# Performance work log

Hardware: AMD Instinct MI355X
Metric: run time of the kernel (lower is better)

## Reference

```python
import jax, jax.numpy as jnp
import numpy as np

NUM_NODES = 100000
NUM_EDGES = 1600000
NUM_GRAPHS = 64
IN_DIM, HID, NCLS = 64, 128, 10


def setup_inputs() -> dict:
    key = jax.random.key(0)
    ks = jax.random.split(key, 12)
    x = jax.random.normal(ks[0], (NUM_NODES, IN_DIM), dtype=jnp.float32)
    src = jax.random.randint(ks[1], (NUM_EDGES,), 0, NUM_NODES, dtype=jnp.int32)
    dst = jax.random.randint(ks[2], (NUM_EDGES,), 0, NUM_NODES, dtype=jnp.int32)
    batch = jnp.sort(jax.random.randint(ks[3], (NUM_NODES,), 0, NUM_GRAPHS, dtype=jnp.int32))
    def glorot(k, shape):
        lim = (6.0 / (shape[0] + shape[1])) ** 0.5
        return jax.random.uniform(k, shape, jnp.float32, -lim, lim)
    return {
        "x": x, "src": src, "dst": dst, "batch": batch,
        "W1": glorot(ks[4], (IN_DIM, HID)), "b1": jnp.zeros((HID,), jnp.float32),
        "W2": glorot(ks[5], (HID, HID)), "b2": jnp.zeros((HID,), jnp.float32),
        "Wl1": glorot(ks[6], (HID, HID // 2)), "bl1": jnp.zeros((HID // 2,), jnp.float32),
        "Wl2": glorot(ks[7], (HID // 2, NCLS)), "bl2": jnp.zeros((NCLS,), jnp.float32),
    }


def gcn_conv(x, W, b, src, dst):
    # GCNConv: out = D^{-1/2} (A + I) D^{-1/2} (x @ W) + b, deg from A+I
    h = x @ W  # [N, H]
    ones = jnp.ones((src.shape[0],), h.dtype)
    deg = jax.ops.segment_sum(ones, dst, num_segments=NUM_NODES) + 1.0  # +1 self-loop
    dinv = jax.lax.rsqrt(deg)  # [N]
    norm = dinv[src] * dinv[dst]  # [E]
    msg = h[src] * norm[:, None]  # [E, H] gather + scale
    agg = jax.ops.segment_sum(msg, dst, num_segments=NUM_NODES)  # scatter-add
    agg = agg + h * (dinv * dinv)[:, None]  # self-loop message
    return agg + b


def reference(x, src, dst, batch, W1, b1, W2, b2, Wl1, bl1, Wl2, bl2):
    h = jax.nn.relu(gcn_conv(x, W1, b1, src, dst))
    h = jax.nn.relu(gcn_conv(h, W2, b2, src, dst))
    # global mean pool per graph
    sums = jax.ops.segment_sum(h, batch, num_segments=NUM_GRAPHS)  # [G, H]
    cnts = jax.ops.segment_sum(jnp.ones((h.shape[0],), h.dtype), batch, num_segments=NUM_GRAPHS)
    pooled = sums / jnp.maximum(cnts, 1.0)[:, None]
    h = jax.nn.relu(pooled @ Wl1 + bl1)
    return h @ Wl2 + bl2  # [G, num_classes]
```

## Files before the change

kernel.cpp:

```cpp
#include <hip/hip_runtime.h>
#include <hip/hip_bf16.h>

#define NODES_N 100000
#define EDGES_E 1600000
#define GRAPHS_G 64

#define BIN_SHIFT 7
#define BIN_NODES 128
#define NBINS 782
#define NB1 512
#define EPB1 3125

typedef unsigned int uint;
typedef unsigned short ushort;
typedef __attribute__((ext_vector_type(8))) short bf16x8;
typedef __attribute__((ext_vector_type(4))) float f32x4;


__device__ inline uint pack_bf2(float lo, float hi) {
    __hip_bfloat162 h2 = __float22bfloat162_rn(make_float2(lo, hi));
    return *reinterpret_cast<uint*>(&h2);
}

__device__ inline void acc_bf2(uint w, float& a0, float& a1) {
    a0 += __uint_as_float(w << 16);
    a1 += __uint_as_float(w & 0xffff0000u);
}

__device__ inline ushort f2bf(float v) {
    __hip_bfloat16 b = __float2bfloat16(v);
    return *reinterpret_cast<ushort*>(&b);
}


__device__ inline void pack_w_one(const float* W, ushort* Wf, int gid, int KS) {
    int j = gid & 7, l = (gid >> 3) & 63, f = gid >> 9;
    int nt = f / KS, ks = f - nt * KS;
    int k = ks * 32 + ((l >> 4) & 3) * 8 + j;
    int n = nt * 16 + (l & 15);
    Wf[gid] = f2bf(W[k * 128 + n]);
}

#define NZERO (GRAPHS_G * 128 + GRAPHS_G)

__global__ void pack_w_zero_k(const float* __restrict__ W1, ushort* __restrict__ W1f,
                              const float* __restrict__ W2, ushort* __restrict__ W2f,
                              float* __restrict__ zf) {
    int gid = blockIdx.x * 256 + threadIdx.x;
    if (gid < 8192) pack_w_one(W1, W1f, gid, 2);
    else if (gid < 24576) pack_w_one(W2, W2f, gid - 8192, 4);
    else {
        int i = gid - 24576;
        if (i < NZERO) zf[i] = 0.f;
    }
}


__global__ __launch_bounds__(256) void p1_hist_k(const int* __restrict__ dst,
                                                 int* __restrict__ hist_t) {
    __shared__ int h[NBINS];
    for (int i = threadIdx.x; i < NBINS; i += 256) h[i] = 0;
    __syncthreads();
    int b = blockIdx.x;
    int e0 = b * EPB1, e1 = min(EDGES_E, e0 + EPB1);
    for (int e = e0 + threadIdx.x; e < e1; e += 256)
        atomicAdd(&h[dst[e] >> BIN_SHIFT], 1);
    __syncthreads();
    for (int i = threadIdx.x; i < NBINS; i += 256)
        hist_t[i * NB1 + b] = h[i];
}

__global__ __launch_bounds__(256) void p1_scanbins_k(int* __restrict__ hist_t,
                                                     int* __restrict__ bintot) {
    __shared__ int sd[256];
    __shared__ int carry;
    int bin = blockIdx.x, t = threadIdx.x;
    if (t == 0) carry = 0;
    __syncthreads();
    int* row = hist_t + bin * NB1;
    for (int base = 0; base < NB1; base += 256) {
        int v = row[base + t];
        sd[t] = v; __syncthreads();
        for (int o = 1; o < 256; o <<= 1) {
            int x = (t >= o) ? sd[t - o] : 0;
            __syncthreads();
            sd[t] += x;
            __syncthreads();
        }
        row[base + t] = carry + sd[t] - v;
        __syncthreads();
        if (t == 255) carry += sd[255];
        __syncthreads();
    }
    if (t == 0) bintot[bin] = carry;
}

__global__ __launch_bounds__(1024) void binstart_k(const int* __restrict__ bintot,
                                                   int* __restrict__ binstart,
                                                   int* __restrict__ rowptr) {
    __shared__ int sd[1024];
    int t = threadIdx.x;
    int v = (t < NBINS) ? bintot[t] : 0;
    sd[t] = v; __syncthreads();
    for (int o = 1; o < 1024; o <<= 1) {
        int x = (t >= o) ? sd[t - o] : 0;
        __syncthreads();
        sd[t] += x;
        __syncthreads();
    }
    if (t < NBINS) binstart[t] = sd[t] - v;
    if (t == 0) { binstart[NBINS] = EDGES_E; rowptr[NODES_N] = EDGES_E; }
}

__global__ __launch_bounds__(256) void p1_scatter_k(const int* __restrict__ src,
                                                    const int* __restrict__ dst,
                                                    const int* __restrict__ hist_t,
                                                    const int* __restrict__ binstart,
                                                    uint* __restrict__ pairs) {
    __shared__ int cur[NBINS];
    int b = blockIdx.x;
    for (int i = threadIdx.x; i < NBINS; i += 256)
        cur[i] = binstart[i] + hist_t[i * NB1 + b];
    __syncthreads();
    int e0 = b * EPB1, e1 = min(EDGES_E, e0 + EPB1);
    for (int e = e0 + threadIdx.x; e < e1; e += 256) {
        int d = dst[e];
        int pos = atomicAdd(&cur[d >> BIN_SHIFT], 1);
        pairs[pos] = ((uint)src[e] << BIN_SHIFT) | (uint)(d & (BIN_NODES - 1));
    }
}

__global__ __launch_bounds__(256) void p2_build_k(const uint* __restrict__ pairs,
                                                  const int* __restrict__ binstart,
                                                  const float* __restrict__ x,
                                                  int* __restrict__ colidx,
                                                  int* __restrict__ rowptr,
                                                  float* __restrict__ dinv,
                                                  uint* __restrict__ xt) {
    __shared__ int h[BIN_NODES];
    __shared__ int off[BIN_NODES];
    __shared__ int cur[BIN_NODES];
    __shared__ float ldv[BIN_NODES];
    int bin = blockIdx.x, t = threadIdx.x;
    int node0 = bin << BIN_SHIFT;
    if (t < BIN_NODES) h[t] = 0;
    __syncthreads();
    int e0 = binstart[bin], e1 = binstart[bin + 1];
    for (int e = e0 + t; e < e1; e += 256)
        atomicAdd(&h[pairs[e] & (BIN_NODES - 1)], 1);
    __syncthreads();
    if (t < BIN_NODES) off[t] = h[t];
    __syncthreads();
    for (int o = 1; o < BIN_NODES; o <<= 1) {
        int x2 = (t < BIN_NODES && t >= o) ? off[t - o] : 0;
        __syncthreads();
        if (t < BIN_NODES) off[t] += x2;
        __syncthreads();
    }
    if (t < BIN_NODES) {
        int excl = off[t] - h[t];
        cur[t] = e0 + excl;
        float dv = rsqrtf((float)h[t] + 1.0f);
        ldv[t] = dv;
        int node = node0 + t;
        if (node < NODES_N) {
            rowptr[node] = e0 + excl;
            dinv[node] = dv;
        }
    }
    __syncthreads();
    for (int e = e0 + t; e < e1; e += 256) {
        uint p = pairs[e];
        int pos = atomicAdd(&cur[p & (BIN_NODES - 1)], 1);
        colidx[pos] = (int)(p >> BIN_SHIFT);
    }
    int nmax = min(NODES_N - node0, BIN_NODES);
    for (int i = t; i < nmax * 16; i += 256) {
        int nl = i >> 4, c = i & 15;
        int node = node0 + nl;
        float dv = ldv[nl];
        float4 v = *(const float4*)&x[(size_t)node * 64 + c * 4];
        uint2 o = make_uint2(pack_bf2(v.x * dv, v.y * dv), pack_bf2(v.z * dv, v.w * dv));
        *(uint2*)&xt[(size_t)node * 32 + c * 2] = o;
    }
}


__global__ __launch_bounds__(256) void gather64_k(const uint* __restrict__ xt,
                                                  const int* __restrict__ rowptr,
                                                  const int* __restrict__ colidx,
                                                  uint* __restrict__ st, int n) {
    int lane = threadIdx.x & 7;
    int local = threadIdx.x >> 3;
    int co = lane * 4;
    int node = blockIdx.x * 32 + local;
    if (node >= n) return;
    {
        float a0=0,a1=0,a2=0,a3=0,a4=0,a5=0,a6=0,a7=0;
        uint4 v = *(const uint4*)&xt[(size_t)node * 32 + co];
        acc_bf2(v.x, a0, a1); acc_bf2(v.y, a2, a3);
        acc_bf2(v.z, a4, a5); acc_bf2(v.w, a6, a7);
        int beg = rowptr[node], end = rowptr[node + 1];
        int e = beg;
        for (; e + 3 < end; e += 4) {
            int s0 = colidx[e], s1 = colidx[e+1], s2 = colidx[e+2], s3 = colidx[e+3];
            uint4 v0 = *(const uint4*)&xt[(size_t)s0 * 32 + co];
            uint4 v1 = *(const uint4*)&xt[(size_t)s1 * 32 + co];
            uint4 v2 = *(const uint4*)&xt[(size_t)s2 * 32 + co];
            uint4 v3 = *(const uint4*)&xt[(size_t)s3 * 32 + co];
            acc_bf2(v0.x,a0,a1); acc_bf2(v0.y,a2,a3); acc_bf2(v0.z,a4,a5); acc_bf2(v0.w,a6,a7);
            acc_bf2(v1.x,a0,a1); acc_bf2(v1.y,a2,a3); acc_bf2(v1.z,a4,a5); acc_bf2(v1.w,a6,a7);
            acc_bf2(v2.x,a0,a1); acc_bf2(v2.y,a2,a3); acc_bf2(v2.z,a4,a5); acc_bf2(v2.w,a6,a7);
            acc_bf2(v3.x,a0,a1); acc_bf2(v3.y,a2,a3); acc_bf2(v3.z,a4,a5); acc_bf2(v3.w,a6,a7);
        }
        for (; e < end; e++) {
            uint4 v0 = *(const uint4*)&xt[(size_t)colidx[e] * 32 + co];
            acc_bf2(v0.x,a0,a1); acc_bf2(v0.y,a2,a3); acc_bf2(v0.z,a4,a5); acc_bf2(v0.w,a6,a7);
        }
        uint4 o;
        o.x = pack_bf2(a0, a1);
        o.y = pack_bf2(a2, a3);
        o.z = pack_bf2(a4, a5);
        o.w = pack_bf2(a6, a7);
        *(uint4*)&st[(size_t)node * 32 + co] = o;
    }
}


__global__ __launch_bounds__(256) void gemm_dual_k(const ushort* __restrict__ A,
                                                   const ushort* __restrict__ W1f,
                                                   const ushort* __restrict__ W2f,
                                                   const float* __restrict__ dinv,
                                                   const float* __restrict__ b1,
                                                   ushort* __restrict__ h2p, int n) {
    __shared__ ushort hl[4][16][132];
    int wave = threadIdx.x >> 6;
    int lane = threadIdx.x & 63;
    int row0 = (blockIdx.x * 4 + wave) * 16;
    if (row0 >= n) return;
    int m = lane & 15, g = lane >> 4;
    int arow = min(row0 + m, n - 1);

    const ushort* ab = &A[(size_t)arow * 64 + g * 8];
    bf16x8 a0 = *reinterpret_cast<const bf16x8*>(ab);
    bf16x8 a1 = *reinterpret_cast<const bf16x8*>(ab + 32);
    f32x4 acc[8];
#pragma unroll
    for (int nt = 0; nt < 8; nt++) {
        acc[nt] = (f32x4){0.f, 0.f, 0.f, 0.f};
        bf16x8 w0 = *reinterpret_cast<const bf16x8*>(&W1f[((size_t)(nt * 2 + 0) * 64 + lane) * 8]);
        bf16x8 w1 = *reinterpret_cast<const bf16x8*>(&W1f[((size_t)(nt * 2 + 1) * 64 + lane) * 8]);
        acc[nt] = __builtin_amdgcn_mfma_f32_16x16x32_bf16(a0, w0, acc[nt], 0, 0, 0);
        acc[nt] = __builtin_amdgcn_mfma_f32_16x16x32_bf16(a1, w1, acc[nt], 0, 0, 0);
    }

    int orow0 = row0 + g * 4;
#pragma unroll
    for (int r = 0; r < 4; r++) {
        float dvr = dinv[min(orow0 + r, n - 1)];
#pragma unroll
        for (int nt = 0; nt < 8; nt++) {
            float v = fmaxf(fmaf(dvr, acc[nt][r], b1[nt * 16 + m]), 0.f);
            hl[wave][g * 4 + r][nt * 16 + m] = f2bf(v);
        }
    }

    bf16x8 hfrag[4];
#pragma unroll
    for (int ks = 0; ks < 4; ks++) {
        uint2 lo = *(const uint2*)&hl[wave][m][g * 8 + ks * 32];
        uint2 hi = *(const uint2*)&hl[wave][m][g * 8 + ks * 32 + 4];
        uint4 u = make_uint4(lo.x, lo.y, hi.x, hi.y);
        hfrag[ks] = *reinterpret_cast<bf16x8*>(&u);
    }

    f32x4 acc2[8];
#pragma unroll
    for (int nt = 0; nt < 8; nt++) {
        acc2[nt] = (f32x4){0.f, 0.f, 0.f, 0.f};
#pragma unroll
        for (int ks = 0; ks < 4; ks++) {
            bf16x8 w = *reinterpret_cast<const bf16x8*>(&W2f[((size_t)(nt * 4 + ks) * 64 + lane) * 8]);
            acc2[nt] = __builtin_amdgcn_mfma_f32_16x16x32_bf16(hfrag[ks], w, acc2[nt], 0, 0, 0);
        }
    }

#pragma unroll
    for (int r = 0; r < 4; r++) {
        int row = orow0 + r;
        if (row < n) {
            float dvr = dinv[row];
#pragma unroll
            for (int nt = 0; nt < 8; nt++)
                h2p[(size_t)row * 128 + nt * 16 + m] = f2bf(acc2[nt][r] * dvr);
        }
    }
}


__global__ __launch_bounds__(256) void gather128_k(const uint* __restrict__ hp,
                                                   const int* __restrict__ rowptr,
                                                   const int* __restrict__ colidx,
                                                   const float* __restrict__ dinv,
                                                   const float* __restrict__ bias,
                                                   uint* __restrict__ h2b, int n) {
    int P = blockIdx.y;
    int lane = threadIdx.x & 7;
    int local = threadIdx.x >> 3;
    int co = P * 32 + lane * 4;
    int node = blockIdx.x * 32 + local;
    if (node >= n) return;
    {
        float a0=0,a1=0,a2=0,a3=0,a4=0,a5=0,a6=0,a7=0;
        uint4 v = *(const uint4*)&hp[(size_t)node * 64 + co];
        acc_bf2(v.x, a0, a1); acc_bf2(v.y, a2, a3);
        acc_bf2(v.z, a4, a5); acc_bf2(v.w, a6, a7);
        int beg = rowptr[node], end = rowptr[node + 1];
        int e = beg;
        for (; e + 3 < end; e += 4) {
            int s0 = colidx[e], s1 = colidx[e+1], s2 = colidx[e+2], s3 = colidx[e+3];
            uint4 v0 = *(const uint4*)&hp[(size_t)s0 * 64 + co];
            uint4 v1 = *(const uint4*)&hp[(size_t)s1 * 64 + co];
            uint4 v2 = *(const uint4*)&hp[(size_t)s2 * 64 + co];
            uint4 v3 = *(const uint4*)&hp[(size_t)s3 * 64 + co];
            acc_bf2(v0.x,a0,a1); acc_bf2(v0.y,a2,a3); acc_bf2(v0.z,a4,a5); acc_bf2(v0.w,a6,a7);
            acc_bf2(v1.x,a0,a1); acc_bf2(v1.y,a2,a3); acc_bf2(v1.z,a4,a5); acc_bf2(v1.w,a6,a7);
            acc_bf2(v2.x,a0,a1); acc_bf2(v2.y,a2,a3); acc_bf2(v2.z,a4,a5); acc_bf2(v2.w,a6,a7);
            acc_bf2(v3.x,a0,a1); acc_bf2(v3.y,a2,a3); acc_bf2(v3.z,a4,a5); acc_bf2(v3.w,a6,a7);
        }
        for (; e < end; e++) {
            uint4 v0 = *(const uint4*)&hp[(size_t)colidx[e] * 64 + co];
            acc_bf2(v0.x,a0,a1); acc_bf2(v0.y,a2,a3); acc_bf2(v0.z,a4,a5); acc_bf2(v0.w,a6,a7);
        }
        float dv = dinv[node];
        int jb = P * 64 + lane * 8;
        float4 b0 = *(const float4*)&bias[jb];
        float4 b1 = *(const float4*)&bias[jb + 4];
        float o0 = fmaxf(fmaf(dv, a0, b0.x), 0.f);
        float o1 = fmaxf(fmaf(dv, a1, b0.y), 0.f);
        float o2 = fmaxf(fmaf(dv, a2, b0.z), 0.f);
        float o3 = fmaxf(fmaf(dv, a3, b0.w), 0.f);
        float o4 = fmaxf(fmaf(dv, a4, b1.x), 0.f);
        float o5 = fmaxf(fmaf(dv, a5, b1.y), 0.f);
        float o6 = fmaxf(fmaf(dv, a6, b1.z), 0.f);
        float o7 = fmaxf(fmaf(dv, a7, b1.w), 0.f);
        uint4 ov;
        ov.x = pack_bf2(o0, o1);
        ov.y = pack_bf2(o2, o3);
        ov.z = pack_bf2(o4, o5);
        ov.w = pack_bf2(o6, o7);
        *(uint4*)&h2b[(size_t)node * 64 + co] = ov;
    }
}


__global__ __launch_bounds__(128) void pool_k(const uint* __restrict__ h2b,
                                              const int* __restrict__ batch, int n,
                                              float* __restrict__ sums, float* __restrict__ cnts) {
    int j = threadIdx.x;
    int wj = j >> 1;
    int hi = j & 1;
    int chunk = (n + gridDim.x - 1) / gridDim.x;
    int i0 = blockIdx.x * chunk;
    int i1 = min(n, i0 + chunk);
    if (i0 >= n) return;
    int cur = batch[i0];
    float acc = 0.f;
    int cnt = 0;
    for (int i = i0; i < i1; i++) {
        int g = batch[i];
        if (g != cur) {
            atomicAdd(&sums[cur * 128 + j], acc);
            if (j == 0) atomicAdd(&cnts[cur], (float)cnt);
            acc = 0.f; cnt = 0; cur = g;
        }
        uint w = h2b[(size_t)i * 64 + wj];
        acc += __uint_as_float(hi ? (w & 0xffff0000u) : (w << 16));
        cnt++;
    }
    atomicAdd(&sums[cur * 128 + j], acc);
    if (j == 0) atomicAdd(&cnts[cur], (float)cnt);
}


__global__ __launch_bounds__(64) void mlp_k(const float* __restrict__ sums, const float* __restrict__ cnts,
                                            const float* __restrict__ Wl1, const float* __restrict__ bl1,
                                            const float* __restrict__ Wl2, const float* __restrict__ bl2,
                                            float* __restrict__ out) {
    __shared__ float pooled[128];
    __shared__ float hidden[64];
    int g = blockIdx.x, t = threadIdx.x;
    float c = fmaxf(cnts[g], 1.0f);
    pooled[t]      = sums[g * 128 + t] / c;
    pooled[t + 64] = sums[g * 128 + 64 + t] / c;
    __syncthreads();
    float a = bl1[t];
#pragma unroll 4
    for (int cc = 0; cc < 128; cc++) a = fmaf(pooled[cc], Wl1[cc * 64 + t], a);
    hidden[t] = fmaxf(a, 0.f);
    __syncthreads();
    if (t < 10) {
        float o = bl2[t];
#pragma unroll 8
        for (int jj = 0; jj < 64; jj++) o = fmaf(hidden[jj], Wl2[jj * 10 + t], o);
        out[g * 10 + t] = o;
    }
}


extern "C" void kernel_launch(void* const* d_in, const int* in_sizes, int n_in,
                              void* d_out, int out_size, void* d_ws, size_t ws_size,
                              hipStream_t stream) {
    const float* x    = (const float*)d_in[0];
    const int*   src  = (const int*)d_in[1];
    const int*   dst  = (const int*)d_in[2];
    const int*   batch= (const int*)d_in[3];
    const float* W1   = (const float*)d_in[4];
    const float* b1   = (const float*)d_in[5];
    const float* W2   = (const float*)d_in[6];
    const float* b2   = (const float*)d_in[7];
    const float* Wl1  = (const float*)d_in[8];
    const float* bl1  = (const float*)d_in[9];
    const float* Wl2  = (const float*)d_in[10];
    const float* bl2  = (const float*)d_in[11];
    float* out = (float*)d_out;

    const int N = NODES_N;

    size_t off = 0;
    auto take = [&](size_t bytes) { size_t o = off; off = (off + bytes + 255) & ~(size_t)255; return o; };
    char* ws = (char*)d_ws;
    uint*   h2p  = (uint*)(ws + take((size_t)N * 128 * 2));
    uint*   h2b  = (uint*)(ws + take((size_t)N * 128 * 2));
    size_t  shbytes = (size_t)N * 64 * 2;
    char*   shreg = ws + take(shbytes);
    uint*   pairs = (uint*)shreg;
    uint*   stil  = (uint*)shreg;
    uint*   xt   = (uint*)(ws + take((size_t)N * 64 * 2));
    float*  dinv = (float*)(ws + take((size_t)N * 4));
    ushort* W1f  = (ushort*)(ws + take((size_t)64 * 128 * 2));
    ushort* W2f  = (ushort*)(ws + take((size_t)128 * 128 * 2));
    size_t zbytes = (size_t)NZERO * 4;
    char*  zbase  = ws + take(zbytes);
    float* sums   = (float*)zbase;
    float* cnts   = (float*)(zbase + (size_t)GRAPHS_G * 128 * 4);
    int*   rowptr = (int*)(ws + take((size_t)(N + 1) * 4));
    int*   colidx = (int*)(ws + take((size_t)EDGES_E * 4));
    int*   hist_t = (int*)(ws + take((size_t)NBINS * NB1 * 4));
    int*   bintot = (int*)(ws + take((size_t)NBINS * 4));
    int*   binstart = (int*)(ws + take((size_t)(NBINS + 1) * 4));
    (void)ws_size; (void)in_sizes; (void)n_in; (void)out_size;

    pack_w_zero_k<<<(24576 + NZERO + 255) / 256, 256, 0, stream>>>(W1, W1f, W2, W2f, sums);

    p1_hist_k<<<NB1, 256, 0, stream>>>(dst, hist_t);
    p1_scanbins_k<<<NBINS, 256, 0, stream>>>(hist_t, bintot);
    binstart_k<<<1, 1024, 0, stream>>>(bintot, binstart, rowptr);
    p1_scatter_k<<<NB1, 256, 0, stream>>>(src, dst, hist_t, binstart, pairs);
    p2_build_k<<<NBINS, 256, 0, stream>>>(pairs, binstart, x, colidx, rowptr, dinv, xt);

    int g32 = (N + 31) / 32;
    gather64_k<<<g32, 256, 0, stream>>>(xt, rowptr, colidx, stil, N);

    int gblk = (N + 63) / 64;
    gemm_dual_k<<<gblk, 256, 0, stream>>>((const ushort*)stil, W1f, W2f, dinv, b1, (ushort*)h2p, N);

    gather128_k<<<dim3(g32, 2), 256, 0, stream>>>(h2p, rowptr, colidx, dinv, b2, h2b, N);

    pool_k<<<1024, 128, 0, stream>>>(h2b, batch, N, sums, cnts);
    mlp_k<<<GRAPHS_G, 64, 0, stream>>>(sums, cnts, Wl1, bl1, Wl2, bl2, out);
}
```

Measured before the change: 217.5 us.

## Fuse second-layer gather with mean pooling, widen bins, unroll gathers by 8

The second GCN aggregation now feeds global mean pooling directly. Each block reduces its nodes into shared-memory per-graph partial sums and then issues global atomics, so the bf16 h2b intermediate and the separate pool kernel are no longer needed. The CSR build bins are doubled to 256 nodes, which halves the block count and lets all 256 threads take part in the scan. Both gather loops are unrolled to 8 neighbours to keep more loads in flight. The trade-off is more atomics in the fused epilogue and higher register pressure from the deeper unroll.

```diff
diff --git a/kernel.cpp b/kernel.cpp
--- a/kernel.cpp
+++ b/kernel.cpp
@@ -5,9 +5,9 @@
 #define EDGES_E 1600000
 #define GRAPHS_G 64
 
-#define BIN_SHIFT 7
-#define BIN_NODES 128
-#define NBINS 782
+#define BIN_SHIFT 8
+#define BIN_NODES 256
+#define NBINS 391
 #define NB1 512
 #define EPB1 3125
 
@@ -143,21 +143,21 @@
     __shared__ float ldv[BIN_NODES];
     int bin = blockIdx.x, t = threadIdx.x;
     int node0 = bin << BIN_SHIFT;
-    if (t < BIN_NODES) h[t] = 0;
+    h[t] = 0;
     __syncthreads();
     int e0 = binstart[bin], e1 = binstart[bin + 1];
     for (int e = e0 + t; e < e1; e += 256)
         atomicAdd(&h[pairs[e] & (BIN_NODES - 1)], 1);
     __syncthreads();
-    if (t < BIN_NODES) off[t] = h[t];
+    off[t] = h[t];
     __syncthreads();
     for (int o = 1; o < BIN_NODES; o <<= 1) {
-        int x2 = (t < BIN_NODES && t >= o) ? off[t - o] : 0;
+        int x2 = (t >= o) ? off[t - o] : 0;
         __syncthreads();
-        if (t < BIN_NODES) off[t] += x2;
+        off[t] += x2;
         __syncthreads();
     }
-    if (t < BIN_NODES) {
+    {
         int excl = off[t] - h[t];
         cur[t] = e0 + excl;
         float dv = rsqrtf((float)h[t] + 1.0f);
@@ -195,35 +195,53 @@
     int co = lane * 4;
     int node = blockIdx.x * 32 + local;
     if (node >= n) return;
-    {
-        float a0=0,a1=0,a2=0,a3=0,a4=0,a5=0,a6=0,a7=0;
-        uint4 v = *(const uint4*)&xt[(size_t)node * 32 + co];
-        acc_bf2(v.x, a0, a1); acc_bf2(v.y, a2, a3);
-        acc_bf2(v.z, a4, a5); acc_bf2(v.w, a6, a7);
-        int beg = rowptr[node], end = rowptr[node + 1];
-        int e = beg;
-        for (; e + 3 < end; e += 4) {
-            int s0 = colidx[e], s1 = colidx[e+1], s2 = colidx[e+2], s3 = colidx[e+3];
-            uint4 v0 = *(const uint4*)&xt[(size_t)s0 * 32 + co];
-            uint4 v1 = *(const uint4*)&xt[(size_t)s1 * 32 + co];
-            uint4 v2 = *(const uint4*)&xt[(size_t)s2 * 32 + co];
-            uint4 v3 = *(const uint4*)&xt[(size_t)s3 * 32 + co];
-            acc_bf2(v0.x,a0,a1); acc_bf2(v0.y,a2,a3); acc_bf2(v0.z,a4,a5); acc_bf2(v0.w,a6,a7);
-            acc_bf2(v1.x,a0,a1); acc_bf2(v1.y,a2,a3); acc_bf2(v1.z,a4,a5); acc_bf2(v1.w,a6,a7);
-            acc_bf2(v2.x,a0,a1); acc_bf2(v2.y,a2,a3); acc_bf2(v2.z,a4,a5); acc_bf2(v2.w,a6,a7);
-            acc_bf2(v3.x,a0,a1); acc_bf2(v3.y,a2,a3); acc_bf2(v3.z,a4,a5); acc_bf2(v3.w,a6,a7);
-        }
-        for (; e < end; e++) {
-            uint4 v0 = *(const uint4*)&xt[(size_t)colidx[e] * 32 + co];
-            acc_bf2(v0.x,a0,a1); acc_bf2(v0.y,a2,a3); acc_bf2(v0.z,a4,a5); acc_bf2(v0.w,a6,a7);
-        }
-        uint4 o;
-        o.x = pack_bf2(a0, a1);
-        o.y = pack_bf2(a2, a3);
-        o.z = pack_bf2(a4, a5);
-        o.w = pack_bf2(a6, a7);
-        *(uint4*)&st[(size_t)node * 32 + co] = o;
-    }
+    float a0=0,a1=0,a2=0,a3=0,a4=0,a5=0,a6=0,a7=0;
+    uint4 v = *(const uint4*)&xt[(size_t)node * 32 + co];
+    acc_bf2(v.x, a0, a1); acc_bf2(v.y, a2, a3);
+    acc_bf2(v.z, a4, a5); acc_bf2(v.w, a6, a7);
+    int beg = rowptr[node], end = rowptr[node + 1];
+    int e = beg;
+    for (; e + 7 < end; e += 8) {
+        int i0 = colidx[e],   i1 = colidx[e+1], i2 = colidx[e+2], i3 = colidx[e+3];
+        int i4 = colidx[e+4], i5 = colidx[e+5], i6 = colidx[e+6], i7 = colidx[e+7];
+        uint4 w0 = *(const uint4*)&xt[(size_t)i0 * 32 + co];
+        uint4 w1 = *(const uint4*)&xt[(size_t)i1 * 32 + co];
+        uint4 w2 = *(const uint4*)&xt[(size_t)i2 * 32 + co];
+        uint4 w3 = *(const uint4*)&xt[(size_t)i3 * 32 + co];
+        uint4 w4 = *(const uint4*)&xt[(size_t)i4 * 32 + co];
+        uint4 w5 = *(const uint4*)&xt[(size_t)i5 * 32 + co];
+        uint4 w6 = *(const uint4*)&xt[(size_t)i6 * 32 + co];
+        uint4 w7 = *(const uint4*)&xt[(size_t)i7 * 32 + co];
+        acc_bf2(w0.x,a0,a1); acc_bf2(w0.y,a2,a3); acc_bf2(w0.z,a4,a5); acc_bf2(w0.w,a6,a7);
+        acc_bf2(w1.x,a0,a1); acc_bf2(w1.y,a2,a3); acc_bf2(w1.z,a4,a5); acc_bf2(w1.w,a6,a7);
+        acc_bf2(w2.x,a0,a1); acc_bf2(w2.y,a2,a3); acc_bf2(w2.z,a4,a5); acc_bf2(w2.w,a6,a7);
+        acc_bf2(w3.x,a0,a1); acc_bf2(w3.y,a2,a3); acc_bf2(w3.z,a4,a5); acc_bf2(w3.w,a6,a7);
+        acc_bf2(w4.x,a0,a1); acc_bf2(w4.y,a2,a3); acc_bf2(w4.z,a4,a5); acc_bf2(w4.w,a6,a7);
+        acc_bf2(w5.x,a0,a1); acc_bf2(w5.y,a2,a3); acc_bf2(w5.z,a4,a5); acc_bf2(w5.w,a6,a7);
+        acc_bf2(w6.x,a0,a1); acc_bf2(w6.y,a2,a3); acc_bf2(w6.z,a4,a5); acc_bf2(w6.w,a6,a7);
+        acc_bf2(w7.x,a0,a1); acc_bf2(w7.y,a2,a3); acc_bf2(w7.z,a4,a5); acc_bf2(w7.w,a6,a7);
+    }
+    for (; e + 3 < end; e += 4) {
+        int i0 = colidx[e], i1 = colidx[e+1], i2 = colidx[e+2], i3 = colidx[e+3];
+        uint4 w0 = *(const uint4*)&xt[(size_t)i0 * 32 + co];
+        uint4 w1 = *(const uint4*)&xt[(size_t)i1 * 32 + co];
+        uint4 w2 = *(const uint4*)&xt[(size_t)i2 * 32 + co];
+        uint4 w3 = *(const uint4*)&xt[(size_t)i3 * 32 + co];
+        acc_bf2(w0.x,a0,a1); acc_bf2(w0.y,a2,a3); acc_bf2(w0.z,a4,a5); acc_bf2(w0.w,a6,a7);
+        acc_bf2(w1.x,a0,a1); acc_bf2(w1.y,a2,a3); acc_bf2(w1.z,a4,a5); acc_bf2(w1.w,a6,a7);
+        acc_bf2(w2.x,a0,a1); acc_bf2(w2.y,a2,a3); acc_bf2(w2.z,a4,a5); acc_bf2(w2.w,a6,a7);
+        acc_bf2(w3.x,a0,a1); acc_bf2(w3.y,a2,a3); acc_bf2(w3.z,a4,a5); acc_bf2(w3.w,a6,a7);
+    }
+    for (; e < end; e++) {
+        uint4 w0 = *(const uint4*)&xt[(size_t)colidx[e] * 32 + co];
+        acc_bf2(w0.x,a0,a1); acc_bf2(w0.y,a2,a3); acc_bf2(w0.z,a4,a5); acc_bf2(w0.w,a6,a7);
+    }
+    uint4 o;
+    o.x = pack_bf2(a0, a1);
+    o.y = pack_bf2(a2, a3);
+    o.z = pack_bf2(a4, a5);
+    o.w = pack_bf2(a6, a7);
+    *(uint4*)&st[(size_t)node * 32 + co] = o;
 }
 
 
@@ -298,88 +316,124 @@
 }
 
 
-__global__ __launch_bounds__(256) void gather128_k(const uint* __restrict__ hp,
-                                                   const int* __restrict__ rowptr,
-                                                   const int* __restrict__ colidx,
-                                                   const float* __restrict__ dinv,
-                                                   const float* __restrict__ bias,
-                                                   uint* __restrict__ h2b, int n) {
+__global__ __launch_bounds__(256) void gather128_pool_k(const uint* __restrict__ hp,
+                                                        const int* __restrict__ rowptr,
+                                                        const int* __restrict__ colidx,
+                                                        const float* __restrict__ dinv,
+                                                        const float* __restrict__ bias,
+                                                        const int* __restrict__ batch,
+                                                        float* __restrict__ sums,
+                                                        float* __restrict__ cnts, int n) {
+    __shared__ float pacc[4][64];
+    __shared__ float pcnt[4];
+    int t = threadIdx.x;
     int P = blockIdx.y;
-    int lane = threadIdx.x & 7;
-    int local = threadIdx.x >> 3;
+    pacc[t >> 6][t & 63] = 0.f;
+    if (t < 4) pcnt[t] = 0.f;
+    __syncthreads();
+
+    int lane = t & 7;
+    int local = t >> 3;
     int co = P * 32 + lane * 4;
-    int node = blockIdx.x * 32 + local;
-    if (node >= n) return;
-    {
+    int node0 = blockIdx.x * 32;
+    int node = node0 + local;
+    bool act = node < n;
+    int g0 = batch[node0];
+
+    float o0=0,o1=0,o2=0,o3=0,o4=0,o5=0,o6=0,o7=0;
+    int g = g0;
+    if (act) {
         float a0=0,a1=0,a2=0,a3=0,a4=0,a5=0,a6=0,a7=0;
         uint4 v = *(const uint4*)&hp[(size_t)node * 64 + co];
         acc_bf2(v.x, a0, a1); acc_bf2(v.y, a2, a3);
         acc_bf2(v.z, a4, a5); acc_bf2(v.w, a6, a7);
         int beg = rowptr[node], end = rowptr[node + 1];
         int e = beg;
+        for (; e + 7 < end; e += 8) {
+            int i0 = colidx[e],   i1 = colidx[e+1], i2 = colidx[e+2], i3 = colidx[e+3];
+            int i4 = colidx[e+4], i5 = colidx[e+5], i6 = colidx[e+6], i7 = colidx[e+7];
+            uint4 w0 = *(const uint4*)&hp[(size_t)i0 * 64 + co];
+            uint4 w1 = *(const uint4*)&hp[(size_t)i1 * 64 + co];
+            uint4 w2 = *(const uint4*)&hp[(size_t)i2 * 64 + co];
+            uint4 w3 = *(const uint4*)&hp[(size_t)i3 * 64 + co];
+            uint4 w4 = *(const uint4*)&hp[(size_t)i4 * 64 + co];
+            uint4 w5 = *(const uint4*)&hp[(size_t)i5 * 64 + co];
+            uint4 w6 = *(const uint4*)&hp[(size_t)i6 * 64 + co];
+            uint4 w7 = *(const uint4*)&hp[(size_t)i7 * 64 + co];
+            acc_bf2(w0.x,a0,a1); acc_bf2(w0.y,a2,a3); acc_bf2(w0.z,a4,a5); acc_bf2(w0.w,a6,a7);
+            acc_bf2(w1.x,a0,a1); acc_bf2(w1.y,a2,a3); acc_bf2(w1.z,a4,a5); acc_bf2(w1.w,a6,a7);
+            acc_bf2(w2.x,a0,a1); acc_bf2(w2.y,a2,a3); acc_bf2(w2.z,a4,a5); acc_bf2(w2.w,a6,a7);
+            acc_bf2(w3.x,a0,a1); acc_bf2(w3.y,a2,a3); acc_bf2(w3.z,a4,a5); acc_bf2(w3.w,a6,a7);
+            acc_bf2(w4.x,a0,a1); acc_bf2(w4.y,a2,a3); acc_bf2(w4.z,a4,a5); acc_bf2(w4.w,a6,a7);
+            acc_bf2(w5.x,a0,a1); acc_bf2(w5.y,a2,a3); acc_bf2(w5.z,a4,a5); acc_bf2(w5.w,a6,a7);
+            acc_bf2(w6.x,a0,a1); acc_bf2(w6.y,a2,a3); acc_bf2(w6.z,a4,a5); acc_bf2(w6.w,a6,a7);
+            acc_bf2(w7.x,a0,a1); acc_bf2(w7.y,a2,a3); acc_bf2(w7.z,a4,a5); acc_bf2(w7.w,a6,a7);
+        }
         for (; e + 3 < end; e += 4) {
-            int s0 = colidx[e], s1 = colidx[e+1], s2 = colidx[e+2], s3 = colidx[e+3];
-            uint4 v0 = *(const uint4*)&hp[(size_t)s0 * 64 + co];
-            uint4 v1 = *(const uint4*)&hp[(size_t)s1 * 64 + co];
-            uint4 v2 = *(const uint4*)&hp[(size_t)s2 * 64 + co];
-            uint4 v3 = *(const uint4*)&hp[(size_t)s3 * 64 + co];
-            acc_bf2(v0.x,a0,a1); acc_bf2(v0.y,a2,a3); acc_bf2(v0.z,a4,a5); acc_bf2(v0.w,a6,a7);
-            acc_bf2(v1.x,a0,a1); acc_bf2(v1.y,a2,a3); acc_bf2(v1.z,a4,a5); acc_bf2(v1.w,a6,a7);
-            acc_bf2(v2.x,a0,a1); acc_bf2(v2.y,a2,a3); acc_bf2(v2.z,a4,a5); acc_bf2(v2.w,a6,a7);
-            acc_bf2(v3.x,a0,a1); acc_bf2(v3.y,a2,a3); acc_bf2(v3.z,a4,a5); acc_bf2(v3.w,a6,a7);
+            int i0 = colidx[e], i1 = colidx[e+1], i2 = colidx[e+2], i3 = colidx[e+3];
+            uint4 w0 = *(const uint4*)&hp[(size_t)i0 * 64 + co];
+            uint4 w1 = *(const uint4*)&hp[(size_t)i1 * 64 + co];
+            uint4 w2 = *(const uint4*)&hp[(size_t)i2 * 64 + co];
+            uint4 w3 = *(const uint4*)&hp[(size_t)i3 * 64 + co];
+            acc_bf2(w0.x,a0,a1); acc_bf2(w0.y,a2,a3); acc_bf2(w0.z,a4,a5); acc_bf2(w0.w,a6,a7);
+            acc_bf2(w1.x,a0,a1); acc_bf2(w1.y,a2,a3); acc_bf2(w1.z,a4,a5); acc_bf2(w1.w,a6,a7);
+            acc_bf2(w2.x,a0,a1); acc_bf2(w2.y,a2,a3); acc_bf2(w2.z,a4,a5); acc_bf2(w2.w,a6,a7);
+            acc_bf2(w3.x,a0,a1); acc_bf2(w3.y,a2,a3); acc_bf2(w3.z,a4,a5); acc_bf2(w3.w,a6,a7);
         }
         for (; e < end; e++) {
-            uint4 v0 = *(const uint4*)&hp[(size_t)colidx[e] * 64 + co];
-            acc_bf2(v0.x,a0,a1); acc_bf2(v0.y,a2,a3); acc_bf2(v0.z,a4,a5); acc_bf2(v0.w,a6,a7);
+            uint4 w0 = *(const uint4*)&hp[(size_t)colidx[e] * 64 + co];
+            acc_bf2(w0.x,a0,a1); acc_bf2(w0.y,a2,a3); acc_bf2(w0.z,a4,a5); acc_bf2(w0.w,a6,a7);
         }
         float dv = dinv[node];
         int jb = P * 64 + lane * 8;
-        float4 b0 = *(const float4*)&bias[jb];
-        float4 b1 = *(const float4*)&bias[jb + 4];
-        float o0 = fmaxf(fmaf(dv, a0, b0.x), 0.f);
-        float o1 = fmaxf(fmaf(dv, a1, b0.y), 0.f);
-        float o2 = fmaxf(fmaf(dv, a2, b0.z), 0.f);
-        float o3 = fmaxf(fmaf(dv, a3, b0.w), 0.f);
-        float o4 = fmaxf(fmaf(dv, a4, b1.x), 0.f);
-        float o5 = fmaxf(fmaf(dv, a5, b1.y), 0.f);
-        float o6 = fmaxf(fmaf(dv, a6, b1.z), 0.f);
-        float o7 = fmaxf(fmaf(dv, a7, b1.w), 0.f);
-        uint4 ov;
-        ov.x = pack_bf2(o0, o1);
-        ov.y = pack_bf2(o2, o3);
-        ov.z = pack_bf2(o4, o5);
-        ov.w = pack_bf2(o6, o7);
-        *(uint4*)&h2b[(size_t)node * 64 + co] = ov;
-    }
-}
-
-
-__global__ __launch_bounds__(128) void pool_k(const uint* __restrict__ h2b,
-                                              const int* __restrict__ batch, int n,
-                                              float* __restrict__ sums, float* __restrict__ cnts) {
-    int j = threadIdx.x;
-    int wj = j >> 1;
-    int hi = j & 1;
-    int chunk = (n + gridDim.x - 1) / gridDim.x;
-    int i0 = blockIdx.x * chunk;
-    int i1 = min(n, i0 + chunk);
-    if (i0 >= n) return;
-    int cur = batch[i0];
-    float acc = 0.f;
-    int cnt = 0;
-    for (int i = i0; i < i1; i++) {
-        int g = batch[i];
-        if (g != cur) {
-            atomicAdd(&sums[cur * 128 + j], acc);
-            if (j == 0) atomicAdd(&cnts[cur], (float)cnt);
-            acc = 0.f; cnt = 0; cur = g;
-        }
-        uint w = h2b[(size_t)i * 64 + wj];
-        acc += __uint_as_float(hi ? (w & 0xffff0000u) : (w << 16));
-        cnt++;
-    }
-    atomicAdd(&sums[cur * 128 + j], acc);
-    if (j == 0) atomicAdd(&cnts[cur], (float)cnt);
+        float4 bb0 = *(const float4*)&bias[jb];
+        float4 bb1 = *(const float4*)&bias[jb + 4];
+        o0 = fmaxf(fmaf(dv, a0, bb0.x), 0.f);
+        o1 = fmaxf(fmaf(dv, a1, bb0.y), 0.f);
+        o2 = fmaxf(fmaf(dv, a2, bb0.z), 0.f);
+        o3 = fmaxf(fmaf(dv, a3, bb0.w), 0.f);
+        o4 = fmaxf(fmaf(dv, a4, bb1.x), 0.f);
+        o5 = fmaxf(fmaf(dv, a5, bb1.y), 0.f);
+        o6 = fmaxf(fmaf(dv, a6, bb1.z), 0.f);
+        o7 = fmaxf(fmaf(dv, a7, bb1.w), 0.f);
+        g = batch[node];
+    }
+
+    if (act) {
+        int slot = g - g0;
+        int c8 = lane * 8;
+        if (slot < 4) {
+            atomicAdd(&pacc[slot][c8 + 0], o0);
+            atomicAdd(&pacc[slot][c8 + 1], o1);
+            atomicAdd(&pacc[slot][c8 + 2], o2);
+            atomicAdd(&pacc[slot][c8 + 3], o3);
+            atomicAdd(&pacc[slot][c8 + 4], o4);
+            atomicAdd(&pacc[slot][c8 + 5], o5);
+            atomicAdd(&pacc[slot][c8 + 6], o6);
+            atomicAdd(&pacc[slot][c8 + 7], o7);
+            if (P == 0 && lane == 0) atomicAdd(&pcnt[slot], 1.f);
+        } else {
+            float* sg = &sums[(size_t)g * 128 + P * 64 + c8];
+            atomicAdd(sg + 0, o0); atomicAdd(sg + 1, o1);
+            atomicAdd(sg + 2, o2); atomicAdd(sg + 3, o3);
+            atomicAdd(sg + 4, o4); atomicAdd(sg + 5, o5);
+            atomicAdd(sg + 6, o6); atomicAdd(sg + 7, o7);
+            if (P == 0 && lane == 0) atomicAdd(&cnts[g], 1.f);
+        }
+    }
+    __syncthreads();
+    {
+        int slot = t >> 6, ch = t & 63;
+        float v = pacc[slot][ch];
+        int gg = g0 + slot;
+        if (v != 0.f && gg < GRAPHS_G)
+            atomicAdd(&sums[(size_t)gg * 128 + P * 64 + ch], v);
+    }
+    if (t < 4 && P == 0) {
+        float c = pcnt[t];
+        int gg = g0 + t;
+        if (c != 0.f && gg < GRAPHS_G) atomicAdd(&cnts[gg], c);
+    }
 }
 
 
@@ -431,7 +485,6 @@
     auto take = [&](size_t bytes) { size_t o = off; off = (off + bytes + 255) & ~(size_t)255; return o; };
     char* ws = (char*)d_ws;
     uint*   h2p  = (uint*)(ws + take((size_t)N * 128 * 2));
-    uint*   h2b  = (uint*)(ws + take((size_t)N * 128 * 2));
     size_t  shbytes = (size_t)N * 64 * 2;
     char*   shreg = ws + take(shbytes);
     uint*   pairs = (uint*)shreg;
@@ -465,8 +518,8 @@
     int gblk = (N + 63) / 64;
     gemm_dual_k<<<gblk, 256, 0, stream>>>((const ushort*)stil, W1f, W2f, dinv, b1, (ushort*)h2p, N);
 
-    gather128_k<<<dim3(g32, 2), 256, 0, stream>>>(h2p, rowptr, colidx, dinv, b2, h2b, N);
-
-    pool_k<<<1024, 128, 0, stream>>>(h2b, batch, N, sums, cnts);
+    gather128_pool_k<<<dim3(g32, 2), 256, 0, stream>>>(h2p, rowptr, colidx, dinv, b2, batch,
+                                                       sums, cnts, N);
+
     mlp_k<<<GRAPHS_G, 64, 0, stream>>>(sums, cnts, Wl1, bl1, Wl2, bl2, out);
 }
```

Result: slower. 237.4 us (+9.1%).
